# Optimization experiments

Measured on AMD Instinct MI355X. Metric: run time of the kernel, lower is better.

## Reference

```python
import jax, jax.numpy as jnp
import numpy as np

PADDING = 4


def _grid_sample_bilinear_zeros(img, grid):
    """torch.nn.functional.grid_sample(img, grid, mode='bilinear',
    padding_mode='zeros', align_corners=False).
    img: [N,C,H,W], grid: [N,Ho,Wo,2] with grid[...,0]=x, grid[...,1]=y in [-1,1].
    """
    N, C, H, W = img.shape
    # unnormalize (align_corners=False)
    ix = ((grid[..., 0] + 1.0) * W - 1.0) * 0.5  # [N,Ho,Wo]
    iy = ((grid[..., 1] + 1.0) * H - 1.0) * 0.5
    x0 = jnp.floor(ix)
    y0 = jnp.floor(iy)
    x1 = x0 + 1.0
    y1 = y0 + 1.0
    wx1 = ix - x0
    wx0 = 1.0 - wx1
    wy1 = iy - y0
    wy0 = 1.0 - wy1

    def tap(yy, xx, w):
        valid = (xx >= 0) & (xx < W) & (yy >= 0) & (yy < H)
        xc = jnp.clip(xx, 0, W - 1).astype(jnp.int32)
        yc = jnp.clip(yy, 0, H - 1).astype(jnp.int32)
        # gather per-sample: v[n,c,i,j] = img[n,c,yc[n,i,j],xc[n,i,j]]
        v = jax.vmap(lambda im, y_, x_: im[:, y_, x_])(img, yc, xc)
        return v * (w * valid)[:, None, :, :]

    return (tap(y0, x0, wy0 * wx0) + tap(y0, x1, wy0 * wx1)
            + tap(y1, x0, wy1 * wx0) + tap(y1, x1, wy1 * wx1))


def setup_inputs() -> dict:
    key = jax.random.key(0)
    k1, k2 = jax.random.split(key)
    N, C, H, W = 512, 9, 84, 84
    x = jax.random.normal(k1, (N, C, H, W), dtype=jnp.float32)
    shift = jax.random.randint(k2, (N, 2), 0, 2 * PADDING + 1, dtype=jnp.int32)
    return {"x": x, "shift": shift}


def reference(x, shift):
    n, c, h, w = x.shape
    p = PADDING
    xp = jnp.pad(x, ((0, 0), (0, 0), (p, p), (p, p)))  # zeros pad
    hp = h + 2 * p
    eps = 1.0 / hp
    arange = jnp.linspace(-1.0 + eps, 1.0 - eps, h, dtype=x.dtype)
    # stack(meshgrid(arange, arange, indexing='ij'), -1): [...,0]=row coord,
    # [...,1]=col coord — fed as-is to grid_sample (matches torch code).
    base = jnp.stack(jnp.meshgrid(arange, arange, indexing='ij'), axis=-1)  # [h,h,2]
    sh = shift.astype(x.dtype) * (2.0 / hp)  # [n,2]
    grid = base[None] + sh[:, None, None, :]  # [n,h,h,2]
    return _grid_sample_bilinear_zeros(xp, grid)
```

## Files before the change

### kernel.cpp

```cpp
#include <hip/hip_runtime.h>


constexpr int HW     = 84;
constexpr int LDSW   = 85;
constexpr int NPLANE = HW * HW;

typedef float vfloat4 __attribute__((ext_vector_type(4)));

__device__ __forceinline__ int iclamp(int v, int lo, int hi) {
    return v < lo ? lo : (v > hi ? hi : v);
}

__global__ __launch_bounds__(256) void rshift_kernel(
    const float* __restrict__ x,
    const int*   __restrict__ shift,
    float*       __restrict__ out)
{
    __shared__ float lds[HW * LDSW];

    const int plane = blockIdx.x;
    const int n     = plane / 9;
    const float s0  = (float)shift[2 * n];
    const float s1  = (float)shift[2 * n + 1];
    const float* __restrict__ src = x   + (size_t)plane * NPLANE;
    float*       __restrict__ dst = out + (size_t)plane * NPLANE;
    const int t = threadIdx.x;
    const float R = 91.0f / 83.0f;

    const int lane = t & 63;
    const int wv   = t >> 6;
    const int jq   = lane % 21;
    const int isub = lane / 21;

    float my0[4], my1[4];
    int   ct0[4], ct1[4];
    #pragma unroll
    for (int e = 0; e < 4; ++e) {
        float fy  = fmaf((float)(4 * jq + e), R, s1);
        int   y0  = (int)fy;
        float wy1 = fy - (float)y0;
        float wy0 = 1.0f - wy1;
        int   t0  = y0 - 4;
        int   t1  = y0 - 3;
        my0[e] = ((unsigned)t0 < 84u) ? wy0 : 0.0f;
        my1[e] = ((unsigned)t1 < 84u) ? wy1 : 0.0f;
        ct0[e] = iclamp(t0, 0, 83);
        ct1[e] = iclamp(t1, 0, 83);
    }

    #pragma unroll
    for (int k = 0; k < 28; ++k) {
        int idx = t + k * 256;
        if (idx < NPLANE) {
            int row = idx / HW;
            int col = idx - row * HW;
            lds[col * LDSW + row] = src[idx];
        }
    }
    __syncthreads();

    if (isub < 3) {
        #pragma unroll
        for (int k = 0; k < 7; ++k) {
            int   i   = k * 12 + wv * 3 + isub;
            float fx  = fmaf((float)i, R, s0);
            int   x0  = (int)fx;
            float wx1 = fx - (float)x0;
            float wx0 = 1.0f - wx1;
            int   u0  = x0 - 4;
            int   u1  = x0 - 3;
            float mx0 = ((unsigned)u0 < 84u) ? wx0 : 0.0f;
            float mx1 = ((unsigned)u1 < 84u) ? wx1 : 0.0f;
            int   cu0 = iclamp(u0, 0, 83) * LDSW;
            int   cu1 = iclamp(u1, 0, 83) * LDSW;

            vfloat4 o;
            #pragma unroll
            for (int e = 0; e < 4; ++e) {
                float v00 = lds[cu0 + ct0[e]];
                float v01 = lds[cu0 + ct1[e]];
                float v10 = lds[cu1 + ct0[e]];
                float v11 = lds[cu1 + ct1[e]];
                o[e] = my0[e] * fmaf(mx0, v00, mx1 * v10)
                     + my1[e] * fmaf(mx0, v01, mx1 * v11);
            }
            __builtin_nontemporal_store(
                o, reinterpret_cast<vfloat4*>(dst + (size_t)i * HW + 4 * jq));
        }
    }
}

extern "C" void kernel_launch(void* const* d_in, const int* in_sizes, int n_in,
                              void* d_out, int out_size, void* d_ws, size_t ws_size,
                              hipStream_t stream) {
    const float* x     = (const float*)d_in[0];
    const int*   shift = (const int*)d_in[1];
    float*       out   = (float*)d_out;
    const int planes = 512 * 9;
    rshift_kernel<<<planes, 256, 0, stream>>>(x, shift, out);
}
```

Measured before the change: 47.51 us.

## Split planes into halves and load tiles via direct global-to-LDS DMA

Each 84x84 plane is now handled by two blocks, each owning a band of output columns and staging only the source rows it needs. The tile is loaded with global_load_lds 16-byte transfers in natural row-major order, replacing the transposed per-element LDS stores. The bilinear taps are rewritten around a single clamped base index with weights remapped at the edges. This doubles the block count for better occupancy and removes VGPR round trips on the load, but it reloads some overlapping rows and relies on the exact LDS placement that global_load_lds produces.

```diff
diff --git a/kernel.cpp b/kernel.cpp
--- a/kernel.cpp
+++ b/kernel.cpp
@@ -1,9 +1,11 @@
 #include <hip/hip_runtime.h>
 
 
-constexpr int HW     = 84;
-constexpr int LDSW   = 85;
+constexpr int HW   = 84;
 constexpr int NPLANE = HW * HW;
+constexpr int NR0  = 53;
+constexpr int NR1  = 40;
+constexpr int LDSD = NR0 * HW;
 
 typedef float vfloat4 __attribute__((ext_vector_type(4)));
 
@@ -16,76 +18,86 @@
     const int*   __restrict__ shift,
     float*       __restrict__ out)
 {
-    __shared__ float lds[HW * LDSW];
+    __shared__ float lds[LDSD];
 
-    const int plane = blockIdx.x;
+    const int bid   = blockIdx.x;
+    const int half  = bid & 1;
+    const int plane = bid >> 1;
     const int n     = plane / 9;
     const float s0  = (float)shift[2 * n];
     const float s1  = (float)shift[2 * n + 1];
-    const float* __restrict__ src = x   + (size_t)plane * NPLANE;
+    const float R   = 91.0f / 83.0f;
+    const int t     = threadIdx.x;
+
+    const int rb = half ? 44 : 0;
+    const int NR = half ? NR1 : NR0;
+    const int NQ = half ? 10 : 11;
+    const int j0 = half ? 44 : 0;
+
+    const float* __restrict__ src = x   + (size_t)plane * NPLANE + rb * HW;
     float*       __restrict__ dst = out + (size_t)plane * NPLANE;
-    const int t = threadIdx.x;
-    const float R = 91.0f / 83.0f;
 
-    const int lane = t & 63;
-    const int wv   = t >> 6;
-    const int jq   = lane % 21;
-    const int isub = lane / 21;
+    const int quads  = NR * (HW / 4);
+    const int wv     = t >> 6;
+    const int rounds = (quads + 255) >> 8;
+    for (int r = 0; r < rounds; ++r) {
+        int lq = t + (r << 8);
+        if (lq < quads) {
+            const float* g = src + lq * 4;
+            __builtin_amdgcn_global_load_lds(
+                (const __attribute__((address_space(1))) float*)g,
+                (__attribute__((address_space(3))) float*)&lds[(r << 10) + (wv << 8)],
+                16, 0, 0);
+        }
+    }
 
-    float my0[4], my1[4];
-    int   ct0[4], ct1[4];
+    const int jq    = t % NQ;
+    const int ibase = t / NQ;
+    float wy0s[4], wy1s[4];
+    int   boff[4];
     #pragma unroll
     for (int e = 0; e < 4; ++e) {
-        float fy  = fmaf((float)(4 * jq + e), R, s1);
-        int   y0  = (int)fy;
-        float wy1 = fy - (float)y0;
-        float wy0 = 1.0f - wy1;
-        int   t0  = y0 - 4;
-        int   t1  = y0 - 3;
-        my0[e] = ((unsigned)t0 < 84u) ? wy0 : 0.0f;
-        my1[e] = ((unsigned)t1 < 84u) ? wy1 : 0.0f;
-        ct0[e] = iclamp(t0, 0, 83);
-        ct1[e] = iclamp(t1, 0, 83);
+        int   j  = j0 + 4 * jq + e;
+        float fy = fmaf((float)j, R, s1);
+        int   y0 = (int)fy;
+        float w1 = fy - (float)y0;
+        float w0 = 1.0f - w1;
+        int   t0 = y0 - 4;
+        int   cb = iclamp(t0, rb, rb + NR - 2);
+        wy0s[e] = (t0 == cb) ? w0 : ((t0 + 1 == cb) ? w1 : 0.0f);
+        wy1s[e] = (t0 == cb) ? w1 : ((t0 - 1 == cb) ? w0 : 0.0f);
+        boff[e] = (cb - rb) * HW;
     }
 
-    #pragma unroll
-    for (int k = 0; k < 28; ++k) {
-        int idx = t + k * 256;
-        if (idx < NPLANE) {
-            int row = idx / HW;
-            int col = idx - row * HW;
-            lds[col * LDSW + row] = src[idx];
-        }
-    }
     __syncthreads();
 
-    if (isub < 3) {
-        #pragma unroll
-        for (int k = 0; k < 7; ++k) {
-            int   i   = k * 12 + wv * 3 + isub;
-            float fx  = fmaf((float)i, R, s0);
-            int   x0  = (int)fx;
-            float wx1 = fx - (float)x0;
-            float wx0 = 1.0f - wx1;
-            int   u0  = x0 - 4;
-            int   u1  = x0 - 3;
-            float mx0 = ((unsigned)u0 < 84u) ? wx0 : 0.0f;
-            float mx1 = ((unsigned)u1 < 84u) ? wx1 : 0.0f;
-            int   cu0 = iclamp(u0, 0, 83) * LDSW;
-            int   cu1 = iclamp(u1, 0, 83) * LDSW;
+    const int ISTEP = half ? 25 : 23;
+    #pragma unroll
+    for (int k = 0; k < 4; ++k) {
+        int i = ibase + k * ISTEP;
+        if (i < HW) {
+            float fx = fmaf((float)i, R, s0);
+            int   x0 = (int)fx;
+            float w1 = fx - (float)x0;
+            float w0 = 1.0f - w1;
+            int   u0 = x0 - 4;
+            int   cb = iclamp(u0, 0, HW - 2);
+            float wx0 = (u0 == cb) ? w0 : ((u0 + 1 == cb) ? w1 : 0.0f);
+            float wx1 = (u0 == cb) ? w1 : ((u0 - 1 == cb) ? w0 : 0.0f);
 
             vfloat4 o;
             #pragma unroll
             for (int e = 0; e < 4; ++e) {
-                float v00 = lds[cu0 + ct0[e]];
-                float v01 = lds[cu0 + ct1[e]];
-                float v10 = lds[cu1 + ct0[e]];
-                float v11 = lds[cu1 + ct1[e]];
-                o[e] = my0[e] * fmaf(mx0, v00, mx1 * v10)
-                     + my1[e] * fmaf(mx0, v01, mx1 * v11);
+                int   b   = boff[e] + cb;
+                float v00 = lds[b];
+                float v10 = lds[b + 1];
+                float v01 = lds[b + HW];
+                float v11 = lds[b + HW + 1];
+                o[e] = wy0s[e] * fmaf(wx0, v00, wx1 * v10)
+                     + wy1s[e] * fmaf(wx0, v01, wx1 * v11);
             }
             __builtin_nontemporal_store(
-                o, reinterpret_cast<vfloat4*>(dst + (size_t)i * HW + 4 * jq));
+                o, reinterpret_cast<vfloat4*>(dst + (size_t)i * HW + j0 + 4 * jq));
         }
     }
 }
@@ -96,6 +108,6 @@
     const float* x     = (const float*)d_in[0];
     const int*   shift = (const int*)d_in[1];
     float*       out   = (float*)d_out;
-    const int planes = 512 * 9;
-    rshift_kernel<<<planes, 256, 0, stream>>>(x, shift, out);
+    const int blocks = 512 * 9 * 2;
+    rshift_kernel<<<blocks, 256, 0, stream>>>(x, shift, out);
 }
```

After: 72.02 us. 51.6% more time.
